# Kernel tuning notes

Hardware: AMD Instinct MI355X
Metric: run time of the kernel (lower is better)

Reference implementation:

```python
import jax, jax.numpy as jnp
import numpy as np

H = 8  # num_heads
NEG = -1e6  # mask fill value used by the torch masked_softmax


def layernorm(x, g, b, eps=1e-5):
    mu = jnp.mean(x, axis=-1, keepdims=True)
    var = jnp.mean(jnp.square(x - mu), axis=-1, keepdims=True)
    return (x - mu) * jax.lax.rsqrt(var + eps) * g + b


def setup_inputs() -> dict:
    key = jax.random.key(0)
    ks = jax.random.split(key, 10)
    B, S, D, F = 8, 1024, 512, 2048
    s = 0.02
    return {
        "X": jax.random.normal(ks[0], (B, S, D), jnp.float32),
        "valid_lens": jax.random.randint(ks[1], (B,), 1, S + 1, jnp.int32),
        "ln1_g": jnp.ones((D,), jnp.float32),
        "ln1_b": jnp.zeros((D,), jnp.float32),
        "Wq": jax.random.normal(ks[2], (D, D), jnp.float32) * s,
        "Wk": jax.random.normal(ks[3], (D, D), jnp.float32) * s,
        "Wv": jax.random.normal(ks[4], (D, D), jnp.float32) * s,
        "Wo": jax.random.normal(ks[5], (D, D), jnp.float32) * s,
        "ln2_g": jnp.ones((D,), jnp.float32),
        "ln2_b": jnp.zeros((D,), jnp.float32),
        "W1": jax.random.normal(ks[6], (D, F), jnp.float32) * s,
        "b1": jnp.zeros((F,), jnp.float32),
        "W2": jax.random.normal(ks[7], (F, D), jnp.float32) * s,
        "b2": jnp.zeros((D,), jnp.float32),
    }


def vit_block(X, valid_lens, ln1_g, ln1_b, Wq, Wk, Wv, Wo, ln2_g, ln2_b, W1, b1, W2, b2):
    B, S, D = X.shape
    dh = D // H
    h = layernorm(X, ln1_g, ln1_b)
    # project and split heads: [B, S, H, dh]
    q = (h @ Wq).reshape(B, S, H, dh)
    k = (h @ Wk).reshape(B, S, H, dh)
    v = (h @ Wv).reshape(B, S, H, dh)
    scores = jnp.einsum("bqhd,bkhd->bhqk", q, k) / jnp.sqrt(jnp.float32(dh))
    # mask keys >= valid_len[b] with -1e6 (as in masked_softmax)
    mask = jnp.arange(S)[None, None, None, :] < valid_lens[:, None, None, None]
    scores = jnp.where(mask, scores, NEG)
    attn = jax.nn.softmax(scores, axis=-1)
    out = jnp.einsum("bhqk,bkhd->bqhd", attn, v).reshape(B, S, D)
    X = X + out @ Wo
    h2 = layernorm(X, ln2_g, ln2_b)
    mlp = jax.nn.gelu(h2 @ W1 + b1, approximate=False) @ W2 + b2
    return X + mlp


def reference(X, valid_lens, ln1_g, ln1_b, Wq, Wk, Wv, Wo, ln2_g, ln2_b, W1, b1, W2, b2):
    return vit_block(X, valid_lens, ln1_g, ln1_b, Wq, Wk, Wv, Wo, ln2_g, ln2_b, W1, b1, W2, b2)
```

## Files before the change

### kernel.cpp

```cpp
#include <hip/hip_runtime.h>
#include <math.h>

#define BB 8
#define SS 1024
#define DD 512
#define FF 2048
#define NH 8
#define MM (BB * SS)
#define LDQKV 1536

using bf8 = __attribute__((ext_vector_type(8))) short;
using f4  = __attribute__((ext_vector_type(4))) float;

#define AS1 __attribute__((address_space(1)))
#define AS3 __attribute__((address_space(3)))

__device__ __forceinline__ void gload16(const void* g, void* l) {
  __builtin_amdgcn_global_load_lds((AS1 const void*)g, (AS3 void*)l, 16, 0, 0);
}

template <int N> __device__ __forceinline__ void wait_vm() {
  if constexpr (N == 0)      asm volatile("s_waitcnt vmcnt(0)" ::: "memory");
  else if constexpr (N == 4) asm volatile("s_waitcnt vmcnt(4)" ::: "memory");
  else if constexpr (N == 6) asm volatile("s_waitcnt vmcnt(6)" ::: "memory");
  else if constexpr (N == 8) asm volatile("s_waitcnt vmcnt(8)" ::: "memory");
  else                       asm volatile("s_waitcnt vmcnt(12)" ::: "memory");
  __builtin_amdgcn_sched_barrier(0);
}

__device__ __forceinline__ void bar() {
  __builtin_amdgcn_sched_barrier(0);
  __builtin_amdgcn_s_barrier();
  __builtin_amdgcn_sched_barrier(0);
}

__device__ __forceinline__ unsigned short f2b(float f) {
  union { float f; unsigned u; } v; v.f = f;
  unsigned r = v.u + 0x7fffu + ((v.u >> 16) & 1u);
  return (unsigned short)(r >> 16);
}

__global__ __launch_bounds__(256) void ln_bf16(const float* __restrict__ x,
                                               const float* __restrict__ g,
                                               const float* __restrict__ bta,
                                               unsigned short* __restrict__ out) {
  int wave = threadIdx.x >> 6, lane = threadIdx.x & 63;
  int row = (blockIdx.x << 2) + wave;
  const float* xr = x + (size_t)row * DD;
  int base = lane << 3;
  float4 v0 = *(const float4*)(xr + base);
  float4 v1 = *(const float4*)(xr + base + 4);
  float s  = v0.x + v0.y + v0.z + v0.w + v1.x + v1.y + v1.z + v1.w;
  float sq = v0.x*v0.x + v0.y*v0.y + v0.z*v0.z + v0.w*v0.w
           + v1.x*v1.x + v1.y*v1.y + v1.z*v1.z + v1.w*v1.w;
  for (int m = 32; m; m >>= 1) { s += __shfl_xor(s, m); sq += __shfl_xor(sq, m); }
  float mu  = s * (1.0f / DD);
  float var = sq * (1.0f / DD) - mu * mu;
  float rs  = rsqrtf(var + 1e-5f);
  float xv[8], go[8], bo[8];
  *(float4*)(xv) = v0; *(float4*)(xv + 4) = v1;
  *(float4*)(go)     = *(const float4*)(g + base);
  *(float4*)(go + 4) = *(const float4*)(g + base + 4);
  *(float4*)(bo)     = *(const float4*)(bta + base);
  *(float4*)(bo + 4) = *(const float4*)(bta + base + 4);
  union { unsigned short u[8]; uint4 v; } ov;
#pragma unroll
  for (int i = 0; i < 8; i++) ov.u[i] = f2b((xv[i] - mu) * rs * go[i] + bo[i]);
  *(uint4*)(out + (size_t)row * DD + base) = ov.v;
}

__global__ __launch_bounds__(256) void tconv(const float* __restrict__ in,
                                             unsigned short* __restrict__ outp,
                                             int K, int N) {
  __shared__ float tile[32][33];
  int n0 = blockIdx.x << 5, k0 = blockIdx.y << 5;
  int c = threadIdx.x & 31, r = threadIdx.x >> 5;
#pragma unroll
  for (int i = 0; i < 4; i++)
    tile[r + 8 * i][c] = in[(size_t)(k0 + r + 8 * i) * N + n0 + c];
  __syncthreads();
#pragma unroll
  for (int i = 0; i < 4; i++)
    outp[(size_t)(n0 + r + 8 * i) * K + k0 + c] = f2b(tile[c][r + 8 * i]);
}

template <int BM, int BN, int ACT>
__global__ __launch_bounds__(256) void gemm_t(
    const unsigned short* __restrict__ A,
    const unsigned short* __restrict__ Bt,
    const float* __restrict__ bias,
    const float* __restrict__ res,
    float* __restrict__ Cf,
    unsigned short* __restrict__ Cb,
    int M, int N, int K) {
  constexpr int WM = BM / 2, WN = BN / 2;
  constexpr int FM = WM / 16, FN = WN / 16;
  constexpr int ACH = BM / 32, BCH = BN / 32;
  constexpr int L = ACH + BCH;
  __shared__ unsigned short As[2][BM * 64];
  __shared__ unsigned short Bs[2][BN * 64];
  int tid = threadIdx.x, wid = tid >> 6, lane = tid & 63;
  int m0 = blockIdx.y * BM, n0 = blockIdx.x * BN;
  int wm = (wid >> 1) * WM, wn = (wid & 1) * WN;
  int r4 = lane & 15, ksl = lane >> 4;
  int srow = lane >> 3, gs = (lane & 7) ^ srow;

  const unsigned short* aBase =
      A + (size_t)(m0 + wid * (ACH * 8) + srow) * K + gs * 8;
  const unsigned short* bBase =
      Bt + (size_t)(n0 + wid * (BCH * 8) + srow) * K + gs * 8;

  f4 acc[FM][FN];
#pragma unroll
  for (int i = 0; i < FM; i++)
#pragma unroll
    for (int j = 0; j < FN; j++) acc[i][j] = (f4){0.f, 0.f, 0.f, 0.f};

  auto STAGE = [&](int buf, int t) {
    int k0 = t << 6;
#pragma unroll
    for (int i = 0; i < ACH; i++)
      gload16(aBase + (size_t)i * 8 * K + k0, &As[buf][(wid * ACH + i) * 512]);
#pragma unroll
    for (int i = 0; i < BCH; i++)
      gload16(bBase + (size_t)i * 8 * K + k0, &Bs[buf][(wid * BCH + i) * 512]);
  };

  auto COMPUTE = [&](int buf) {
#pragma unroll
    for (int k2 = 0; k2 < 2; k2++) {
      bf8 af[FM], bfr[FN];
#pragma unroll
      for (int mi = 0; mi < FM; mi++) {
        int r = wm + mi * 16 + r4;
        af[mi] = *(const bf8*)((const char*)&As[buf][0] + r * 128 +
                               (((k2 * 4 + ksl) ^ (r & 7)) << 4));
      }
#pragma unroll
      for (int ni = 0; ni < FN; ni++) {
        int r = wn + ni * 16 + r4;
        bfr[ni] = *(const bf8*)((const char*)&Bs[buf][0] + r * 128 +
                                (((k2 * 4 + ksl) ^ (r & 7)) << 4));
      }
#pragma unroll
      for (int mi = 0; mi < FM; mi++)
#pragma unroll
        for (int ni = 0; ni < FN; ni++)
          acc[mi][ni] = __builtin_amdgcn_mfma_f32_16x16x32_bf16(
              af[mi], bfr[ni], acc[mi][ni], 0, 0, 0);
    }
  };

  int nt = K >> 6;
  STAGE(0, 0);
  STAGE(1, 1);
  for (int t = 0; t < nt; t++) {
    if (t + 1 < nt) wait_vm<L>();
    else            wait_vm<0>();
    bar();
    COMPUTE(t & 1);
    bar();
    if (t + 2 < nt) STAGE(t & 1, t + 2);
  }

  int rq = (lane >> 4) << 2;
#pragma unroll
  for (int ni = 0; ni < FN; ni++) {
    int col = n0 + wn + ni * 16 + r4;
    float bv = bias ? bias[col] : 0.0f;
#pragma unroll
    for (int mi = 0; mi < FM; mi++) {
#pragma unroll
      for (int j = 0; j < 4; j++) {
        int row = m0 + wm + mi * 16 + rq + j;
        float v = acc[mi][ni][j] + bv;
        if (ACT) v = 0.5f * v * (1.0f + erff(v * 0.70710678118654752f));
        if (res) v += res[(size_t)row * N + col];
        if (Cf) Cf[(size_t)row * N + col] = v;
        else    Cb[(size_t)row * N + col] = f2b(v);
      }
    }
  }
}

__global__ __launch_bounds__(256) void attn_mfma(
    const unsigned short* __restrict__ QKV,
    const int* __restrict__ vlen,
    unsigned short* __restrict__ AO) {
  __shared__ unsigned short Qs[64 * 64];
  __shared__ unsigned short Ks[64 * 64];
  __shared__ unsigned short Vt[64 * 64];
  __shared__ unsigned short Ps[64 * 64];
  int b = blockIdx.z, h = blockIdx.y, q0 = blockIdx.x << 6;
  int tid = threadIdx.x, wid = tid >> 6, lane = tid & 63;
  int vl = vlen[b];
  int r4 = lane & 15, ksl = lane >> 4;

  int srow = lane >> 3;
  int gs = (lane & 7) ^ srow;
  {
    const unsigned short* qsrc =
        QKV + (size_t)(b * SS + q0 + wid * 16 + srow) * LDQKV + h * 64 + gs * 8;
    gload16(qsrc, Qs + wid * 1024);
    gload16(qsrc + (size_t)8 * LDQKV, Qs + wid * 1024 + 512);
  }
  const unsigned short* kbase =
      QKV + (size_t)(b * SS + wid * 16 + srow) * LDQKV + DD + h * 64 + gs * 8;
  int vp = tid & 31, vdg = (tid >> 5) << 3;
  const unsigned short* vbase =
      QKV + (size_t)(b * SS + 2 * vp) * LDQKV + 2 * DD + h * 64 + vdg;

  f4 o[4];
#pragma unroll
  for (int i = 0; i < 4; i++) o[i] = (f4){0.f, 0.f, 0.f, 0.f};
  float mrun[4], lrun[4];
#pragma unroll
  for (int j = 0; j < 4; j++) { mrun[j] = -3e38f; lrun[j] = 0.0f; }

  int ntiles = (vl + 63) >> 6;
  if (ntiles > 16) ntiles = 16;

  for (int t = 0; t < ntiles; t++) {
    int kg0 = t << 6;
    const unsigned short* ks = kbase + (size_t)kg0 * LDQKV;
    gload16(ks, Ks + wid * 1024);
    gload16(ks + (size_t)8 * LDQKV, Ks + wid * 1024 + 512);
    {
      const unsigned short* v0 = vbase + (size_t)kg0 * LDQKV;
      const unsigned short* v1 = v0 + LDQKV;
      unsigned short va[8], vb[8];
      *(uint4*)va = *(const uint4*)v0;
      *(uint4*)vb = *(const uint4*)v1;
#pragma unroll
      for (int i = 0; i < 8; i++) {
        int d = vdg + i;
        unsigned val = (unsigned)va[i] | ((unsigned)vb[i] << 16);
        int byte = (d << 7) + (((vp >> 2) ^ (d & 7)) << 4) + ((vp & 3) << 2);
        *(unsigned*)((char*)Vt + byte) = val;
      }
    }
    __syncthreads();

    f4 s[4];
#pragma unroll
    for (int i = 0; i < 4; i++) s[i] = (f4){0.f, 0.f, 0.f, 0.f};
#pragma unroll
    for (int k2 = 0; k2 < 2; k2++) {
      int slot = (k2 << 2) + ksl;
      int qr = (wid << 4) + r4;
      bf8 aq = *(const bf8*)((const char*)Qs + (qr << 7) + ((slot ^ (qr & 7)) << 4));
#pragma unroll
      for (int ni = 0; ni < 4; ni++) {
        int kr = (ni << 4) + r4;
        bf8 bk = *(const bf8*)((const char*)Ks + (kr << 7) + ((slot ^ (kr & 7)) << 4));
        s[ni] = __builtin_amdgcn_mfma_f32_16x16x32_bf16(aq, bk, s[ni], 0, 0, 0);
      }
    }

#pragma unroll
    for (int j = 0; j < 4; j++) {
      int qr = (wid << 4) + ((lane >> 4) << 2) + j;
      float sv[4], mx = -3e38f;
#pragma unroll
      for (int ni = 0; ni < 4; ni++) {
        float v = s[ni][j] * 0.125f;
        if (kg0 + (ni << 4) + r4 >= vl) v = -1e6f;
        sv[ni] = v;
        mx = fmaxf(mx, v);
      }
#pragma unroll
      for (int m2 = 1; m2 < 16; m2 <<= 1) mx = fmaxf(mx, __shfl_xor(mx, m2));
      float mnew = fmaxf(mrun[j], mx);
      float al = __expf(mrun[j] - mnew);
      float ls = 0.0f;
      unsigned short pb[4];
#pragma unroll
      for (int ni = 0; ni < 4; ni++) {
        float p = __expf(sv[ni] - mnew);
        ls += p;
        pb[ni] = f2b(p);
      }
#pragma unroll
      for (int m2 = 1; m2 < 16; m2 <<= 1) ls += __shfl_xor(ls, m2);
      lrun[j] = lrun[j] * al + ls;
      mrun[j] = mnew;
#pragma unroll
      for (int ni = 0; ni < 4; ni++) {
        int kc = (ni << 4) + r4;
        int byte = (qr << 7) + (((kc >> 3) ^ (qr & 7)) << 4) + ((kc & 7) << 1);
        *(unsigned short*)((char*)Ps + byte) = pb[ni];
        o[ni][j] *= al;
      }
    }

#pragma unroll
    for (int k2 = 0; k2 < 2; k2++) {
      int slot = (k2 << 2) + ksl;
      int qr = (wid << 4) + r4;
      bf8 ap = *(const bf8*)((const char*)Ps + (qr << 7) + ((slot ^ (qr & 7)) << 4));
#pragma unroll
      for (int ni = 0; ni < 4; ni++) {
        int dr = (ni << 4) + r4;
        bf8 bv = *(const bf8*)((const char*)Vt + (dr << 7) + ((slot ^ (dr & 7)) << 4));
        o[ni] = __builtin_amdgcn_mfma_f32_16x16x32_bf16(ap, bv, o[ni], 0, 0, 0);
      }
    }
    __syncthreads();
  }

  float inv[4];
#pragma unroll
  for (int j = 0; j < 4; j++) inv[j] = 1.0f / lrun[j];
#pragma unroll
  for (int ni = 0; ni < 4; ni++) {
#pragma unroll
    for (int j = 0; j < 4; j++) {
      int qr = (wid << 4) + ((lane >> 4) << 2) + j;
      int d = (ni << 4) + r4;
      AO[(size_t)(b * SS + q0 + qr) * DD + h * 64 + d] = f2b(o[ni][j] * inv[j]);
    }
  }
}

extern "C" void kernel_launch(void* const* d_in, const int* in_sizes, int n_in,
                              void* d_out, int out_size, void* d_ws,
                              size_t ws_size, hipStream_t stream) {
  const float* X    = (const float*)d_in[0];
  const int*   vln  = (const int*)d_in[1];
  const float* ln1g = (const float*)d_in[2];
  const float* ln1b = (const float*)d_in[3];
  const float* Wq   = (const float*)d_in[4];
  const float* Wk   = (const float*)d_in[5];
  const float* Wv   = (const float*)d_in[6];
  const float* Wo   = (const float*)d_in[7];
  const float* ln2g = (const float*)d_in[8];
  const float* ln2b = (const float*)d_in[9];
  const float* W1   = (const float*)d_in[10];
  const float* b1   = (const float*)d_in[11];
  const float* W2   = (const float*)d_in[12];
  const float* b2   = (const float*)d_in[13];
  float* out = (float*)d_out;

  unsigned short* ws = (unsigned short*)d_ws;
  unsigned short* h     = ws;
  unsigned short* QKVb  = h     + (size_t)MM * DD;
  unsigned short* AOb   = QKVb  + (size_t)MM * LDQKV;
  unsigned short* mid   = AOb   + (size_t)MM * DD;
  unsigned short* Wqkvt = mid   + (size_t)MM * FF;
  unsigned short* Wot   = Wqkvt + (size_t)3 * DD * DD;
  unsigned short* W1t   = Wot   + (size_t)DD * DD;
  unsigned short* W2t   = W1t   + (size_t)FF * DD;

  dim3 blk(256);

  tconv<<<dim3(16, 16), blk, 0, stream>>>(Wq, Wqkvt, DD, DD);
  tconv<<<dim3(16, 16), blk, 0, stream>>>(Wk, Wqkvt + (size_t)DD * DD, DD, DD);
  tconv<<<dim3(16, 16), blk, 0, stream>>>(Wv, Wqkvt + (size_t)2 * DD * DD, DD, DD);
  tconv<<<dim3(16, 16), blk, 0, stream>>>(Wo, Wot, DD, DD);
  tconv<<<dim3(64, 16), blk, 0, stream>>>(W1, W1t, DD, FF);
  tconv<<<dim3(16, 64), blk, 0, stream>>>(W2, W2t, FF, DD);

  ln_bf16<<<dim3(MM / 4), blk, 0, stream>>>(X, ln1g, ln1b, h);
  gemm_t<128, 128, 0><<<dim3(LDQKV / 128, MM / 128), blk, 0, stream>>>(
      h, Wqkvt, nullptr, nullptr, nullptr, QKVb, MM, LDQKV, DD);
  attn_mfma<<<dim3(SS / 64, NH, BB), blk, 0, stream>>>(QKVb, vln, AOb);
  gemm_t<128, 64, 0><<<dim3(DD / 64, MM / 128), blk, 0, stream>>>(
      AOb, Wot, nullptr, X, out, nullptr, MM, DD, DD);
  ln_bf16<<<dim3(MM / 4), blk, 0, stream>>>(out, ln2g, ln2b, h);
  gemm_t<128, 128, 1><<<dim3(FF / 128, MM / 128), blk, 0, stream>>>(
      h, W1t, b1, nullptr, nullptr, mid, MM, FF, DD);
  gemm_t<128, 64, 0><<<dim3(DD / 64, MM / 128), blk, 0, stream>>>(
      mid, W2t, b2, out, out, nullptr, MM, DD, FF);
}
```

Measured before the change: 211.9 us.

## Retune GEMM: K=32 tiles, block swizzle, transposed MFMA, vector epilogue, fast GELU

The GEMM now uses a 32-wide K tile with halved LDS and a new XOR swizzle, and asks for 4 blocks per CU through launch bounds. It remaps a 1D grid in groups of 8 for L2 locality and swaps the MFMA operand order so each lane holds 4 consecutive columns. That lets the epilogue use float4 bias, residual and output accesses. It also replaces erff with an Abramowitz-Stegun erf approximation (about 1e-7 error) and merges four weight transpose launches into one. The risks are more barriers per K, register pressure under the occupancy hint, and the small GELU accuracy change.

```diff
diff --git a/kernel.cpp b/kernel.cpp
--- a/kernel.cpp
+++ b/kernel.cpp
@@ -21,10 +21,10 @@
 
 template <int N> __device__ __forceinline__ void wait_vm() {
   if constexpr (N == 0)      asm volatile("s_waitcnt vmcnt(0)" ::: "memory");
+  else if constexpr (N == 3) asm volatile("s_waitcnt vmcnt(3)" ::: "memory");
   else if constexpr (N == 4) asm volatile("s_waitcnt vmcnt(4)" ::: "memory");
   else if constexpr (N == 6) asm volatile("s_waitcnt vmcnt(6)" ::: "memory");
-  else if constexpr (N == 8) asm volatile("s_waitcnt vmcnt(8)" ::: "memory");
-  else                       asm volatile("s_waitcnt vmcnt(12)" ::: "memory");
+  else                       asm volatile("s_waitcnt vmcnt(8)" ::: "memory");
   __builtin_amdgcn_sched_barrier(0);
 }
 
@@ -38,6 +38,18 @@
   union { float f; unsigned u; } v; v.f = f;
   unsigned r = v.u + 0x7fffu + ((v.u >> 16) & 1u);
   return (unsigned short)(r >> 16);
+}
+
+__device__ __forceinline__ float gelu_f(float x) {
+  float ax = fabsf(x) * 0.70710678118654752f;
+  float t = 1.0f / (1.0f + 0.3275911f * ax);
+  float poly = t * (0.254829592f +
+               t * (-0.284496736f +
+               t * (1.421413741f +
+               t * (-1.453152027f + t * 1.061405429f))));
+  float erfv = 1.0f - poly * __expf(-ax * ax);
+  erfv = copysignf(erfv, x);
+  return 0.5f * x * (1.0f + erfv);
 }
 
 __global__ __launch_bounds__(256) void ln_bf16(const float* __restrict__ x,
@@ -84,74 +96,101 @@
     outp[(size_t)(n0 + r + 8 * i) * K + k0 + c] = f2b(tile[c][r + 8 * i]);
 }
 
+__global__ __launch_bounds__(256) void tconv4(
+    const float* __restrict__ s0, const float* __restrict__ s1,
+    const float* __restrict__ s2, const float* __restrict__ s3,
+    unsigned short* __restrict__ d0, unsigned short* __restrict__ d1,
+    unsigned short* __restrict__ d2, unsigned short* __restrict__ d3) {
+  __shared__ float tile[32][33];
+  const float* in; unsigned short* outp;
+  switch (blockIdx.z) {
+    case 0: in = s0; outp = d0; break;
+    case 1: in = s1; outp = d1; break;
+    case 2: in = s2; outp = d2; break;
+    default: in = s3; outp = d3; break;
+  }
+  int n0 = blockIdx.x << 5, k0 = blockIdx.y << 5;
+  int c = threadIdx.x & 31, r = threadIdx.x >> 5;
+#pragma unroll
+  for (int i = 0; i < 4; i++)
+    tile[r + 8 * i][c] = in[(size_t)(k0 + r + 8 * i) * DD + n0 + c];
+  __syncthreads();
+#pragma unroll
+  for (int i = 0; i < 4; i++)
+    outp[(size_t)(n0 + r + 8 * i) * DD + k0 + c] = f2b(tile[c][r + 8 * i]);
+}
+
 template <int BM, int BN, int ACT>
-__global__ __launch_bounds__(256) void gemm_t(
+__global__ __launch_bounds__(256, 4) void gemm_t(
     const unsigned short* __restrict__ A,
     const unsigned short* __restrict__ Bt,
     const float* __restrict__ bias,
     const float* __restrict__ res,
     float* __restrict__ Cf,
     unsigned short* __restrict__ Cb,
-    int M, int N, int K) {
+    int M, int N, int K, int gx) {
   constexpr int WM = BM / 2, WN = BN / 2;
   constexpr int FM = WM / 16, FN = WN / 16;
-  constexpr int ACH = BM / 32, BCH = BN / 32;
+  constexpr int ACH = BM / 64, BCH = BN / 64;
   constexpr int L = ACH + BCH;
-  __shared__ unsigned short As[2][BM * 64];
-  __shared__ unsigned short Bs[2][BN * 64];
+  __shared__ unsigned short As[2][BM * 32];
+  __shared__ unsigned short Bs[2][BN * 32];
   int tid = threadIdx.x, wid = tid >> 6, lane = tid & 63;
-  int m0 = blockIdx.y * BM, n0 = blockIdx.x * BN;
+
+  int bid = blockIdx.x;
+  int cpx = (int)gridDim.x >> 3;
+  int swz = (bid & 7) * cpx + (bid >> 3);
+  int m0 = (swz / gx) * BM, n0 = (swz % gx) * BN;
+
   int wm = (wid >> 1) * WM, wn = (wid & 1) * WN;
   int r4 = lane & 15, ksl = lane >> 4;
-  int srow = lane >> 3, gs = (lane & 7) ^ srow;
+  int srow = lane >> 2;
+  int gs = (lane & 3) ^ ((lane >> 3) & 3);
 
   const unsigned short* aBase =
-      A + (size_t)(m0 + wid * (ACH * 8) + srow) * K + gs * 8;
+      A + (size_t)(m0 + wid * (ACH * 16) + srow) * K + gs * 8;
   const unsigned short* bBase =
-      Bt + (size_t)(n0 + wid * (BCH * 8) + srow) * K + gs * 8;
-
-  f4 acc[FM][FN];
-#pragma unroll
-  for (int i = 0; i < FM; i++)
-#pragma unroll
-    for (int j = 0; j < FN; j++) acc[i][j] = (f4){0.f, 0.f, 0.f, 0.f};
+      Bt + (size_t)(n0 + wid * (BCH * 16) + srow) * K + gs * 8;
+
+  f4 acc[FN][FM];
+#pragma unroll
+  for (int i = 0; i < FN; i++)
+#pragma unroll
+    for (int j = 0; j < FM; j++) acc[i][j] = (f4){0.f, 0.f, 0.f, 0.f};
 
   auto STAGE = [&](int buf, int t) {
-    int k0 = t << 6;
+    int k0 = t << 5;
 #pragma unroll
     for (int i = 0; i < ACH; i++)
-      gload16(aBase + (size_t)i * 8 * K + k0, &As[buf][(wid * ACH + i) * 512]);
+      gload16(aBase + (size_t)i * 16 * K + k0, &As[buf][(wid * ACH + i) * 512]);
 #pragma unroll
     for (int i = 0; i < BCH; i++)
-      gload16(bBase + (size_t)i * 8 * K + k0, &Bs[buf][(wid * BCH + i) * 512]);
+      gload16(bBase + (size_t)i * 16 * K + k0, &Bs[buf][(wid * BCH + i) * 512]);
   };
 
   auto COMPUTE = [&](int buf) {
-#pragma unroll
-    for (int k2 = 0; k2 < 2; k2++) {
-      bf8 af[FM], bfr[FN];
-#pragma unroll
-      for (int mi = 0; mi < FM; mi++) {
-        int r = wm + mi * 16 + r4;
-        af[mi] = *(const bf8*)((const char*)&As[buf][0] + r * 128 +
-                               (((k2 * 4 + ksl) ^ (r & 7)) << 4));
-      }
-#pragma unroll
-      for (int ni = 0; ni < FN; ni++) {
-        int r = wn + ni * 16 + r4;
-        bfr[ni] = *(const bf8*)((const char*)&Bs[buf][0] + r * 128 +
-                                (((k2 * 4 + ksl) ^ (r & 7)) << 4));
-      }
+    bf8 af[FM], bfr[FN];
+#pragma unroll
+    for (int mi = 0; mi < FM; mi++) {
+      int r = wm + mi * 16 + r4;
+      af[mi] = *(const bf8*)((const char*)&As[buf][0] + r * 64 +
+                             ((ksl ^ ((r >> 1) & 3)) << 4));
+    }
+#pragma unroll
+    for (int ni = 0; ni < FN; ni++) {
+      int r = wn + ni * 16 + r4;
+      bfr[ni] = *(const bf8*)((const char*)&Bs[buf][0] + r * 64 +
+                              ((ksl ^ ((r >> 1) & 3)) << 4));
+    }
+#pragma unroll
+    for (int ni = 0; ni < FN; ni++)
 #pragma unroll
       for (int mi = 0; mi < FM; mi++)
-#pragma unroll
-        for (int ni = 0; ni < FN; ni++)
-          acc[mi][ni] = __builtin_amdgcn_mfma_f32_16x16x32_bf16(
-              af[mi], bfr[ni], acc[mi][ni], 0, 0, 0);
-    }
+        acc[ni][mi] = __builtin_amdgcn_mfma_f32_16x16x32_bf16(
+            bfr[ni], af[mi], acc[ni][mi], 0, 0, 0);
   };
 
-  int nt = K >> 6;
+  int nt = K >> 5;
   STAGE(0, 0);
   STAGE(1, 1);
   for (int t = 0; t < nt; t++) {
@@ -166,18 +205,29 @@
   int rq = (lane >> 4) << 2;
 #pragma unroll
   for (int ni = 0; ni < FN; ni++) {
-    int col = n0 + wn + ni * 16 + r4;
-    float bv = bias ? bias[col] : 0.0f;
+    int col = n0 + wn + ni * 16 + rq;
+    float bv[4] = {0.f, 0.f, 0.f, 0.f};
+    if (bias) *(float4*)bv = *(const float4*)(bias + col);
 #pragma unroll
     for (int mi = 0; mi < FM; mi++) {
+      int row = m0 + wm + mi * 16 + r4;
+      float v[4];
 #pragma unroll
       for (int j = 0; j < 4; j++) {
-        int row = m0 + wm + mi * 16 + rq + j;
-        float v = acc[mi][ni][j] + bv;
-        if (ACT) v = 0.5f * v * (1.0f + erff(v * 0.70710678118654752f));
-        if (res) v += res[(size_t)row * N + col];
-        if (Cf) Cf[(size_t)row * N + col] = v;
-        else    Cb[(size_t)row * N + col] = f2b(v);
+        v[j] = acc[ni][mi][j] + bv[j];
+        if (ACT) v[j] = gelu_f(v[j]);
+      }
+      if (res) {
+        float4 rv = *(const float4*)(res + (size_t)row * N + col);
+        v[0] += rv.x; v[1] += rv.y; v[2] += rv.z; v[3] += rv.w;
+      }
+      if (Cf) {
+        *(float4*)(Cf + (size_t)row * N + col) = *(float4*)v;
+      } else {
+        union { unsigned short u[4]; uint2 q; } p;
+#pragma unroll
+        for (int j = 0; j < 4; j++) p.u[j] = f2b(v[j]);
+        *(uint2*)(Cb + (size_t)row * N + col) = p.q;
       }
     }
   }
@@ -353,22 +403,21 @@
 
   dim3 blk(256);
 
-  tconv<<<dim3(16, 16), blk, 0, stream>>>(Wq, Wqkvt, DD, DD);
-  tconv<<<dim3(16, 16), blk, 0, stream>>>(Wk, Wqkvt + (size_t)DD * DD, DD, DD);
-  tconv<<<dim3(16, 16), blk, 0, stream>>>(Wv, Wqkvt + (size_t)2 * DD * DD, DD, DD);
-  tconv<<<dim3(16, 16), blk, 0, stream>>>(Wo, Wot, DD, DD);
+  tconv4<<<dim3(16, 16, 4), blk, 0, stream>>>(
+      Wq, Wk, Wv, Wo, Wqkvt, Wqkvt + (size_t)DD * DD,
+      Wqkvt + (size_t)2 * DD * DD, Wot);
   tconv<<<dim3(64, 16), blk, 0, stream>>>(W1, W1t, DD, FF);
   tconv<<<dim3(16, 64), blk, 0, stream>>>(W2, W2t, FF, DD);
 
   ln_bf16<<<dim3(MM / 4), blk, 0, stream>>>(X, ln1g, ln1b, h);
-  gemm_t<128, 128, 0><<<dim3(LDQKV / 128, MM / 128), blk, 0, stream>>>(
-      h, Wqkvt, nullptr, nullptr, nullptr, QKVb, MM, LDQKV, DD);
+  gemm_t<128, 128, 0><<<dim3((LDQKV / 128) * (MM / 128)), blk, 0, stream>>>(
+      h, Wqkvt, nullptr, nullptr, nullptr, QKVb, MM, LDQKV, DD, LDQKV / 128);
   attn_mfma<<<dim3(SS / 64, NH, BB), blk, 0, stream>>>(QKVb, vln, AOb);
-  gemm_t<128, 64, 0><<<dim3(DD / 64, MM / 128), blk, 0, stream>>>(
-      AOb, Wot, nullptr, X, out, nullptr, MM, DD, DD);
+  gemm_t<128, 64, 0><<<dim3((DD / 64) * (MM / 128)), blk, 0, stream>>>(
+      AOb, Wot, nullptr, X, out, nullptr, MM, DD, DD, DD / 64);
   ln_bf16<<<dim3(MM / 4), blk, 0, stream>>>(out, ln2g, ln2b, h);
-  gemm_t<128, 128, 1><<<dim3(FF / 128, MM / 128), blk, 0, stream>>>(
-      h, W1t, b1, nullptr, nullptr, mid, MM, FF, DD);
-  gemm_t<128, 64, 0><<<dim3(DD / 64, MM / 128), blk, 0, stream>>>(
-      mid, W2t, b2, out, out, nullptr, MM, DD, FF);
-}
+  gemm_t<128, 128, 1><<<dim3((FF / 128) * (MM / 128)), blk, 0, stream>>>(
+      h, W1t, b1, nullptr, nullptr, mid, MM, FF, DD, FF / 128);
+  gemm_t<128, 64, 0><<<dim3((DD / 64) * (MM / 128)), blk, 0, stream>>>(
+      mid, W2t, b2, out, out, nullptr, MM, DD, FF, DD / 64);
+}
```

After: 179.4 us. 1.18x faster.
